# Kernel optimization log

Measured on AMD Instinct MI355X. Metric: run time of the kernel, lower is better.

The kernel has to match this reference:

```python
import jax, jax.numpy as jnp
import numpy as np

B, N, IN_DIM, OUT_DIM, H = 4, 2048, 128, 128, 4
NEG_SLOPE = 0.2


def setup_inputs() -> dict:
    key = jax.random.key(0)
    ks = jax.random.split(key, 6)
    # Xavier-ish scaling for stable softmax logits
    node_features = jax.random.normal(ks[0], (B, N, IN_DIM), dtype=jnp.float32)
    adjacency = jax.random.randint(ks[1], (B, N, N), 0, 2, dtype=jnp.int32)
    W = jax.random.normal(ks[2], (H, IN_DIM, OUT_DIM), dtype=jnp.float32) / np.sqrt(IN_DIM)
    a = jax.random.normal(ks[3], (H, 2 * OUT_DIM), dtype=jnp.float32) / np.sqrt(2 * OUT_DIM)
    out_proj_w = jax.random.normal(ks[4], (H * OUT_DIM, OUT_DIM), dtype=jnp.float32) / np.sqrt(H * OUT_DIM)
    out_proj_b = jax.random.normal(ks[5], (OUT_DIM,), dtype=jnp.float32) * 0.01
    return {"node_features": node_features, "adjacency": adjacency, "W": W,
            "a": a, "out_proj_w": out_proj_w, "out_proj_b": out_proj_b}


def reference(node_features, adjacency, W, a, out_proj_w, out_proj_b):
    D = W.shape[-1]
    # Per-head projection: h[b,h,n,o]
    h = jnp.einsum('bni,hio->bhno', node_features, W)
    # Additive attention score a^T [h_i || h_j] decomposed into src+dst parts
    # (exact since the score Linear has no bias).
    s = jnp.einsum('bhno,ho->bhn', h, a[:, :D])   # contribution of h_i
    d = jnp.einsum('bhno,ho->bhn', h, a[:, D:])   # contribution of h_j
    e = jax.nn.leaky_relu(s[..., :, None] + d[..., None, :], NEG_SLOPE)  # [B,H,N,N]
    e = jnp.where(adjacency[:, None, :, :] == 0, -jnp.inf, e)
    alpha = jax.nn.softmax(e, axis=-1)                                   # [B,H,N,N]
    out = jnp.einsum('bhnm,bhmo->bhno', alpha, h)                        # [B,H,N,D]
    b, nh, n, _ = out.shape
    cat = out.transpose(0, 2, 1, 3).reshape(b, n, nh * D)                # concat heads
    output = cat @ out_proj_w + out_proj_b                               # [B,N,D]
    return output, alpha
```

## Files before the change

kernel.cpp:

```cpp
#include <hip/hip_runtime.h>
#include <hip/hip_bf16.h>

#define BB 4
#define NN 2048
#define DD 128
#define HH 4
#define LOG2E 1.4426950408889634f
#define NEG_BIG (-1e30f)

typedef __attribute__((ext_vector_type(8))) short bf16x8;
typedef __attribute__((ext_vector_type(4))) short bf16x4;
typedef __attribute__((ext_vector_type(4))) float f32x4;
typedef __attribute__((ext_vector_type(8))) _Float16 f16x8;
typedef __attribute__((ext_vector_type(4))) _Float16 f16x4;

__device__ __forceinline__ unsigned short f2bf(float f) {
    union { float f; unsigned int u; } v; v.f = f;
    unsigned int r = v.u + 0x7FFF + ((v.u >> 16) & 1);
    return (unsigned short)(r >> 16);
}

__global__ __launch_bounds__(128) void k_prep(const float* __restrict__ W,
                                              const float* __restrict__ a,
                                              float* __restrict__ wsv,
                                              float* __restrict__ wdv,
                                              _Float16* __restrict__ WT16) {
    int h = blockIdx.x;
    int i = threadIdx.x;
    const float* Wr  = W + (h * DD + i) * DD;
    const float* as_ = a + h * 2 * DD;
    const float* ad_ = as_ + DD;
    float s = 0.f, d = 0.f;
    for (int o = 0; o < DD; ++o) {
        float w = Wr[o];
        s += w * as_[o];
        d += w * ad_[o];
        WT16[((size_t)h * DD + o) * DD + i] = (_Float16)w;
    }
    wsv[h * DD + i] = s;
    wdv[h * DD + i] = d;
}

__global__ __launch_bounds__(256) void k_sd(const float* __restrict__ x,
                                            const float* __restrict__ wsv,
                                            const float* __restrict__ wdv,
                                            float* __restrict__ s_out,
                                            float* __restrict__ d_out_) {
    __shared__ float xs[64 * 129];
    __shared__ float ws[4 * 129], wd[4 * 129];
    int tid = threadIdx.x;
    int b  = blockIdx.x / (NN / 64);
    int nb = (blockIdx.x % (NN / 64)) * 64;
    for (int idx = tid; idx < HH * DD; idx += 256) {
        ws[(idx >> 7) * 129 + (idx & 127)] = wsv[idx];
        wd[(idx >> 7) * 129 + (idx & 127)] = wdv[idx];
    }
    for (int idx = tid; idx < 64 * 128; idx += 256) {
        int r = idx >> 7, c = idx & 127;
        xs[r * 129 + c] = x[((size_t)b * NN + nb + r) * DD + c];
    }
    __syncthreads();
    int h = tid & 3, r = tid >> 2;
    float sv = 0.f, dv = 0.f;
#pragma unroll 8
    for (int i = 0; i < DD; ++i) {
        float xv = xs[r * 129 + i];
        sv += xv * ws[h * 129 + i];
        dv += xv * wd[h * 129 + i];
    }
    int n = nb + r;
    s_out[(b * HH + h) * NN + n] = sv;
    d_out_[(b * HH + h) * NN + n] = dv;
}

__global__ __launch_bounds__(256) void k_h_mfma(const float* __restrict__ x,
                                                const _Float16* __restrict__ WT16,
                                                unsigned short* __restrict__ hT) {
    __shared__ unsigned short wt_lds[128 * 128];
    __shared__ unsigned short x_lds[64 * 128];
    int tid = threadIdx.x;
    int bh = blockIdx.x >> 5;
    int nb = (blockIdx.x & 31) * 64;
    int b = bh >> 2, h = bh & 3;

    {
        int o = tid >> 1, ihalf = (tid & 1) * 64;
        const _Float16* src = WT16 + ((size_t)h * DD + o) * DD + ihalf;
#pragma unroll
        for (int q = 0; q < 8; ++q) {
            f16x8 v = *(const f16x8*)(src + q * 8);
            int byte = ((ihalf + q * 8) * 2) ^ ((o & 15) << 4);
            *(f16x8*)&wt_lds[o * 128 + (byte >> 1)] = v;
        }
    }
    {
        int n = tid >> 2, iseg = (tid & 3) * 32;
        const float* src = x + ((size_t)b * NN + nb + n) * DD + iseg;
#pragma unroll
        for (int q = 0; q < 8; ++q) {
            float4 v = *(const float4*)(src + q * 4);
            f16x4 p;
            p[0] = (_Float16)v.x; p[1] = (_Float16)v.y;
            p[2] = (_Float16)v.z; p[3] = (_Float16)v.w;
            int byte = ((iseg + q * 4) * 2) ^ ((n & 15) << 4);
            *(f16x4*)&x_lds[n * 128 + (byte >> 1)] = p;
        }
    }
    __syncthreads();

    int l = tid & 63, w = tid >> 6, col = l & 15, quad = l >> 4;
    f32x4 acc[8];
#pragma unroll
    for (int ot = 0; ot < 8; ++ot) acc[ot] = (f32x4){0.f, 0.f, 0.f, 0.f};
#pragma unroll
    for (int k = 0; k < 4; ++k) {
        int cbyte = (k * 64 + quad * 16) ^ (col << 4);
        f16x8 bv = *(const f16x8*)&x_lds[(w * 16 + col) * 128 + (cbyte >> 1)];
#pragma unroll
        for (int ot = 0; ot < 8; ++ot) {
            f16x8 av = *(const f16x8*)&wt_lds[(ot * 16 + col) * 128 + (cbyte >> 1)];
            acc[ot] = __builtin_amdgcn_mfma_f32_16x16x32_f16(av, bv, acc[ot], 0, 0, 0);
        }
    }
    unsigned short* base = hT + (size_t)bh * DD * NN;
#pragma unroll
    for (int ot = 0; ot < 8; ++ot)
#pragma unroll
        for (int r = 0; r < 4; ++r)
            base[(size_t)(ot * 16 + quad * 4 + r) * NN + nb + w * 16 + col] =
                f2bf(acc[ot][r]);
}

__global__ __launch_bounds__(256) void k_dmax(const float* __restrict__ d_,
                                              float* __restrict__ dmax_) {
    __shared__ float red[4];
    int bh = blockIdx.x, tid = threadIdx.x;
    const float4* dp = (const float4*)(d_ + (size_t)bh * NN);
    float4 v0 = dp[tid];
    float4 v1 = dp[256 + tid];
    float m = fmaxf(fmaxf(fmaxf(v0.x, v0.y), fmaxf(v0.z, v0.w)),
                    fmaxf(fmaxf(v1.x, v1.y), fmaxf(v1.z, v1.w)));
#pragma unroll
    for (int off = 32; off >= 1; off >>= 1)
        m = fmaxf(m, __shfl_xor(m, off, 64));
    if ((tid & 63) == 0) red[tid >> 6] = m;
    __syncthreads();
    if (tid == 0)
        dmax_[bh] = fmaxf(fmaxf(red[0], red[1]), fmaxf(red[2], red[3]));
}

struct AdjD {
    int4   a4[8];
    float4 d4;
};

__device__ __forceinline__ void adjd_load(int mb, const int* adj_base,
                                          const float* dg, int ac4, AdjD& R) {
#pragma unroll
    for (int p = 0; p < 8; ++p)
        R.a4[p] = *(const int4*)(adj_base + (size_t)(p * 8) * NN + mb);
    R.d4 = *(const float4*)(dg + mb + ac4);
}

__device__ __forceinline__ void p1_accum(const AdjD& R, const float (&sreg)[8],
                                         const float (&Mreg)[8], float (&Lp)[8]) {
#pragma unroll
    for (int p = 0; p < 8; ++p) {
        float sn = sreg[p], Mn = Mreg[p];
        float t0 = sn + R.d4.x, t1 = sn + R.d4.y;
        float t2 = sn + R.d4.z, t3 = sn + R.d4.w;
        float v0 = t0 > 0.f ? t0 : 0.2f * t0;
        float v1 = t1 > 0.f ? t1 : 0.2f * t1;
        float v2 = t2 > 0.f ? t2 : 0.2f * t2;
        float v3 = t3 > 0.f ? t3 : 0.2f * t3;
        float e0 = (R.a4[p].x != 0) ? exp2f((v0 - Mn) * LOG2E) : 0.f;
        float e1 = (R.a4[p].y != 0) ? exp2f((v1 - Mn) * LOG2E) : 0.f;
        float e2 = (R.a4[p].z != 0) ? exp2f((v2 - Mn) * LOG2E) : 0.f;
        float e3 = (R.a4[p].w != 0) ? exp2f((v3 - Mn) * LOG2E) : 0.f;
        Lp[p] += (e0 + e1) + (e2 + e3);
    }
}

template <bool WRITE_ALPHA>
__device__ __forceinline__ void attn_tile_body(
    int mb, AdjD& cur, AdjD& nxt,
    const int* adj_base, const float* dg, int ac4,
    const unsigned short* hbase,
    unsigned short* al_lds, unsigned short* hT_lds,
    const float (&sreg)[8], const float (&Mreg)[8], const float (&Lin)[8],
    float* alpha_base, int ar0, int hrow0, int hbyte,
    int w, int col, int quad, f32x4 (&acc)[8])
{
    bf16x8 hv[8];
#pragma unroll
    for (int q = 0; q < 8; ++q)
        hv[q] = *(const bf16x8*)(hbase + (size_t)(q * 16) * NN + mb);
    adjd_load((mb + 128) & (NN - 1), adj_base, dg, ac4, nxt);

#pragma unroll
    for (int p = 0; p < 8; ++p) {
        int row = p * 8 + ar0;
        float sn = sreg[p], Mn = Mreg[p], Li = Lin[p];
        float t0 = sn + cur.d4.x, t1 = sn + cur.d4.y;
        float t2 = sn + cur.d4.z, t3 = sn + cur.d4.w;
        float v0 = t0 > 0.f ? t0 : 0.2f * t0;
        float v1 = t1 > 0.f ? t1 : 0.2f * t1;
        float v2 = t2 > 0.f ? t2 : 0.2f * t2;
        float v3 = t3 > 0.f ? t3 : 0.2f * t3;
        float e0 = (cur.a4[p].x != 0) ? exp2f((v0 - Mn) * LOG2E) * Li : 0.f;
        float e1 = (cur.a4[p].y != 0) ? exp2f((v1 - Mn) * LOG2E) * Li : 0.f;
        float e2 = (cur.a4[p].z != 0) ? exp2f((v2 - Mn) * LOG2E) * Li : 0.f;
        float e3 = (cur.a4[p].w != 0) ? exp2f((v3 - Mn) * LOG2E) * Li : 0.f;
        bf16x4 pk;
        pk[0] = (short)f2bf(e0); pk[1] = (short)f2bf(e1);
        pk[2] = (short)f2bf(e2); pk[3] = (short)f2bf(e3);
        int abyte = (ac4 * 2) ^ ((row & 15) << 4);
        *(bf16x4*)&al_lds[row * 128 + (abyte >> 1)] = pk;
        if (WRITE_ALPHA) {
            float4 ev; ev.x = e0; ev.y = e1; ev.z = e2; ev.w = e3;
            *(float4*)(alpha_base + (size_t)(p * 8) * NN + mb) = ev;
        }
    }
#pragma unroll
    for (int q = 0; q < 8; ++q)
        *(bf16x8*)&hT_lds[(q * 16 + hrow0) * 128 + (hbyte >> 1)] = hv[q];

    __syncthreads();
#pragma unroll
    for (int k = 0; k < 4; ++k) {
        int cbyte = (k * 64 + quad * 16) ^ (col << 4);
        bf16x8 af = *(const bf16x8*)&al_lds[(w * 16 + col) * 128 + (cbyte >> 1)];
#pragma unroll
        for (int ot = 0; ot < 8; ++ot) {
            bf16x8 bfv = *(const bf16x8*)&hT_lds[(ot * 16 + col) * 128 + (cbyte >> 1)];
            acc[ot] = __builtin_amdgcn_mfma_f32_16x16x32_bf16(af, bfv, acc[ot], 0, 0, 0);
        }
    }
    __syncthreads();
}

template <bool WRITE_ALPHA>
__global__ __launch_bounds__(256) void k_attn_mfma(const int* __restrict__ adj,
                                                   const float* __restrict__ s_in,
                                                   const float* __restrict__ d_in_,
                                                   const float* __restrict__ dmax_,
                                                   const unsigned short* __restrict__ hT,
                                                   float* __restrict__ out_scr,
                                                   float* __restrict__ alpha_out,
                                                   float* __restrict__ Li_out) {
    __shared__ unsigned short al_lds[64 * 128];
    __shared__ unsigned short hT_lds[128 * 128];
    int tid = threadIdx.x;
    int bid = (int)(blockIdx.x & 7) * 64 + (int)(blockIdx.x >> 3);
    int bh = bid >> 5;
    int nb = (bid & 31) * 64;
    int b = bh >> 2;

    int ar0 = tid >> 5;
    int ac4 = (tid & 31) * 4;
    const int* adj_base = adj + ((size_t)b * NN + nb + ar0) * NN + ac4;
    float* alpha_base = WRITE_ALPHA
        ? alpha_out + ((size_t)bh * NN + nb + ar0) * NN + ac4 : nullptr;
    const float* dg = d_in_ + (size_t)bh * NN;

    float dmx = dmax_[bh];
    float sreg[8], Mreg[8];
#pragma unroll
    for (int p = 0; p < 8; ++p) {
        sreg[p] = s_in[bh * NN + nb + p * 8 + ar0];
        float t = sreg[p] + dmx;
        Mreg[p] = t > 0.f ? t : 0.2f * t;
    }

    float Lp[8];
#pragma unroll
    for (int p = 0; p < 8; ++p) Lp[p] = 0.f;
    {
        AdjD A0, A1;
        adjd_load(0, adj_base, dg, ac4, A0);
        for (int mb = 0; mb < NN; mb += 256) {
            adjd_load(mb + 128, adj_base, dg, ac4, A1);
            p1_accum(A0, sreg, Mreg, Lp);
            adjd_load((mb + 256) & (NN - 1), adj_base, dg, ac4, A0);
            p1_accum(A1, sreg, Mreg, Lp);
        }
    }
#pragma unroll
    for (int off = 16; off >= 1; off >>= 1)
#pragma unroll
        for (int p = 0; p < 8; ++p)
            Lp[p] += __shfl_xor(Lp[p], off, 64);
    float Lin[8];
#pragma unroll
    for (int p = 0; p < 8; ++p) Lin[p] = Lp[p] > 0.f ? 1.f / Lp[p] : 0.f;
    if (!WRITE_ALPHA && (tid & 31) == 0) {
#pragma unroll
        for (int p = 0; p < 8; ++p)
            Li_out[bh * NN + nb + p * 8 + ar0] = Lin[p];
    }

    int hrow0 = tid >> 4;
    int hcolu = (tid & 15) * 8;
    const unsigned short* hbase = hT + ((size_t)bh * DD + hrow0) * NN + hcolu;
    int hbyte = (hcolu * 2) ^ (hrow0 << 4);
    int l = tid & 63, w = tid >> 6, col = l & 15, quad = l >> 4;

    f32x4 acc[8];
#pragma unroll
    for (int ot = 0; ot < 8; ++ot) acc[ot] = (f32x4){0.f, 0.f, 0.f, 0.f};

    AdjD A0, A1;
    adjd_load(0, adj_base, dg, ac4, A0);

    for (int mb = 0; mb < NN; mb += 256) {
        attn_tile_body<WRITE_ALPHA>(mb, A0, A1, adj_base, dg, ac4, hbase,
                                    al_lds, hT_lds, sreg, Mreg, Lin,
                                    alpha_base, ar0, hrow0, hbyte,
                                    w, col, quad, acc);
        attn_tile_body<WRITE_ALPHA>(mb + 128, A1, A0, adj_base, dg, ac4, hbase,
                                    al_lds, hT_lds, sreg, Mreg, Lin,
                                    alpha_base, ar0, hrow0, hbyte,
                                    w, col, quad, acc);
    }
#pragma unroll
    for (int ot = 0; ot < 8; ++ot)
#pragma unroll
        for (int r = 0; r < 4; ++r)
            out_scr[((size_t)bh * NN + nb + w * 16 + quad * 4 + r) * DD + ot * 16 + col] =
                acc[ot][r];
}

__global__ __launch_bounds__(256) void k_proj(const float* __restrict__ out_scr,
                                              const float* __restrict__ Wp,
                                              const float* __restrict__ bias,
                                              float* __restrict__ out) {
    __shared__ float cs[16 * 512];
    int tid = threadIdx.x;
    int b  = blockIdx.x / (NN / 16);
    int nb = (blockIdx.x % (NN / 16)) * 16;
    for (int idx = tid; idx < 16 * 512; idx += 256) {
        int r = idx >> 9, c = idx & 511;
        int hh = c >> 7, oo = c & 127;
        cs[idx] = out_scr[((size_t)(b * HH + hh) * NN + nb + r) * DD + oo];
    }
    __syncthreads();
    int o = tid & 63, rg = tid >> 6;
    float bv0 = bias[o], bv1 = bias[o + 64];
    float acc0[4], acc1[4];
#pragma unroll
    for (int j = 0; j < 4; ++j) { acc0[j] = bv0; acc1[j] = bv1; }
    for (int k = 0; k < 512; k += 4) {
        float w00 = Wp[(k + 0) * DD + o], w01 = Wp[(k + 0) * DD + o + 64];
        float w10 = Wp[(k + 1) * DD + o], w11 = Wp[(k + 1) * DD + o + 64];
        float w20 = Wp[(k + 2) * DD + o], w21 = Wp[(k + 2) * DD + o + 64];
        float w30 = Wp[(k + 3) * DD + o], w31 = Wp[(k + 3) * DD + o + 64];
#pragma unroll
        for (int j = 0; j < 4; ++j) {
            float4 cq = *(const float4*)&cs[(rg * 4 + j) * 512 + k];
            acc0[j] += cq.x * w00 + cq.y * w10 + cq.z * w20 + cq.w * w30;
            acc1[j] += cq.x * w01 + cq.y * w11 + cq.z * w21 + cq.w * w31;
        }
    }
#pragma unroll
    for (int j = 0; j < 4; ++j) {
        out[((size_t)b * NN + nb + rg * 4 + j) * DD + o]      = acc0[j];
        out[((size_t)b * NN + nb + rg * 4 + j) * DD + o + 64] = acc1[j];
    }
}

__global__ __launch_bounds__(256) void k_alpha(const int* __restrict__ adj,
                                               const float* __restrict__ s_in,
                                               const float* __restrict__ d_in_,
                                               const float* __restrict__ dmax_,
                                               const float* __restrict__ Li_in,
                                               float* __restrict__ alpha_out) {
    int tid = threadIdx.x;
    int b = blockIdx.x / NN, n = blockIdx.x % NN;
    float sv[4], Mv[4], Lv[4];
#pragma unroll
    for (int h = 0; h < 4; ++h) {
        sv[h] = s_in[(b * HH + h) * NN + n];
        float t = sv[h] + dmax_[b * HH + h];
        Mv[h] = t > 0.f ? t : 0.2f * t;
        Lv[h] = Li_in[(b * HH + h) * NN + n];
    }
    const int* arow = adj + ((size_t)b * NN + n) * NN;
    for (int m = tid; m < NN; m += 256) {
        int av = arow[m];
#pragma unroll
        for (int h = 0; h < 4; ++h) {
            float val = 0.f;
            if (av != 0) {
                float t = sv[h] + d_in_[(b * HH + h) * NN + m];
                float v = t > 0.f ? t : 0.2f * t;
                val = exp2f((v - Mv[h]) * LOG2E) * Lv[h];
            }
            alpha_out[((size_t)(b * HH + h) * NN + n) * NN + m] = val;
        }
    }
}

extern "C" void kernel_launch(void* const* d_in, const int* in_sizes, int n_in,
                              void* d_out, int out_size, void* d_ws, size_t ws_size,
                              hipStream_t stream) {
    const float* x    = (const float*)d_in[0];
    const int*   adj  = (const int*)d_in[1];
    const float* W    = (const float*)d_in[2];
    const float* a    = (const float*)d_in[3];
    const float* Wp   = (const float*)d_in[4];
    const float* bias = (const float*)d_in[5];

    float* out       = (float*)d_out;
    float* alpha_out = out + (size_t)BB * NN * DD;

    float* ws    = (float*)d_ws;
    float* wsv   = ws;
    float* wdv   = wsv + HH * DD;
    float* s_    = wdv + HH * DD;
    float* d_    = s_ + (size_t)BB * HH * NN;
    float* Li_   = d_ + (size_t)BB * HH * NN;
    float* dmax_ = Li_ + (size_t)BB * HH * NN;
    _Float16* WT16 = (_Float16*)(dmax_ + 16);

    const size_t stats_bytes = (2 * HH * DD + 3 * (size_t)BB * HH * NN + 16) * sizeof(float)
                             + (size_t)HH * DD * DD * sizeof(_Float16);
    const size_t hT_bytes    = (size_t)BB * HH * NN * DD * sizeof(unsigned short);
    const size_t scr_bytes   = (size_t)BB * HH * NN * DD * sizeof(float);
    const bool fused = ws_size >= stats_bytes + hT_bytes + scr_bytes;

    unsigned short* hT;
    float* out_scr;
    if (fused) {
        hT      = (unsigned short*)((char*)d_ws + stats_bytes);
        out_scr = (float*)((char*)hT + hT_bytes);
    } else {
        hT      = (unsigned short*)alpha_out;
        out_scr = alpha_out + (size_t)BB * HH * NN * DD;
    }

    k_prep<<<HH, 128, 0, stream>>>(W, a, wsv, wdv, WT16);
    k_sd<<<BB * NN / 64, 256, 0, stream>>>(x, wsv, wdv, s_, d_);
    k_h_mfma<<<BB * HH * (NN / 64), 256, 0, stream>>>(x, WT16, hT);
    k_dmax<<<BB * HH, 256, 0, stream>>>(d_, dmax_);
    if (fused) {
        k_attn_mfma<true><<<BB * HH * (NN / 64), 256, 0, stream>>>(adj, s_, d_, dmax_,
                                                                   hT, out_scr, alpha_out, Li_);
        k_proj<<<BB * (NN / 16), 256, 0, stream>>>(out_scr, Wp, bias, out);
    } else {
        k_attn_mfma<false><<<BB * HH * (NN / 64), 256, 0, stream>>>(adj, s_, d_, dmax_,
                                                                    hT, out_scr, alpha_out, Li_);
        k_proj<<<BB * (NN / 16), 256, 0, stream>>>(out_scr, Wp, bias, out);
        k_alpha<<<BB * NN, 256, 0, stream>>>(adj, s_, d_, dmax_, Li_, alpha_out);
    }
}
```

Measured before the change: 444.7 us.

## Pack adjacency into bitmask once and read bits in attention kernel

Adds a pre-pass kernel that compresses the int32 adjacency matrix into one bit per entry, stored in workspace. The attention kernel's two passes (row-sum and alpha/MFMA) then read 32-bit mask words instead of int4 adjacency vectors, cutting the adjacency traffic that was previously read once per head and per pass. This costs one extra full read of the adjacency plus a small bitmask write, and a larger workspace requirement, which could drop the path into the non-fused fallback if the workspace is too small.

```diff
diff --git a/kernel.cpp b/kernel.cpp
--- a/kernel.cpp
+++ b/kernel.cpp
@@ -41,6 +41,22 @@
     wdv[h * DD + i] = d;
 }
 
+__global__ __launch_bounds__(256) void k_mask(const int* __restrict__ adj,
+                                              unsigned int* __restrict__ mbits) {
+    size_t w = (size_t)blockIdx.x * 256 + threadIdx.x;
+    const int* src = adj + w * 32;
+    unsigned int m = 0;
+#pragma unroll
+    for (int q = 0; q < 8; ++q) {
+        int4 a = *(const int4*)(src + q * 4);
+        m |= (a.x != 0 ? 1u : 0u) << (q * 4 + 0);
+        m |= (a.y != 0 ? 1u : 0u) << (q * 4 + 1);
+        m |= (a.z != 0 ? 1u : 0u) << (q * 4 + 2);
+        m |= (a.w != 0 ? 1u : 0u) << (q * 4 + 3);
+    }
+    mbits[w] = m;
+}
+
 __global__ __launch_bounds__(256) void k_sd(const float* __restrict__ x,
                                             const float* __restrict__ wsv,
                                             const float* __restrict__ wdv,
@@ -149,42 +165,45 @@
         dmax_[bh] = fmaxf(fmaxf(red[0], red[1]), fmaxf(red[2], red[3]));
 }
 
-struct AdjD {
-    int4   a4[8];
+struct MaskD {
+    unsigned int mw[8];
     float4 d4;
 };
 
-__device__ __forceinline__ void adjd_load(int mb, const int* adj_base,
-                                          const float* dg, int ac4, AdjD& R) {
+__device__ __forceinline__ void maskd_load(int mb, const unsigned int* mask_base,
+                                           const float* dg, int ac4, MaskD& R) {
+    int wo = mb >> 5;
 #pragma unroll
     for (int p = 0; p < 8; ++p)
-        R.a4[p] = *(const int4*)(adj_base + (size_t)(p * 8) * NN + mb);
+        R.mw[p] = mask_base[(size_t)(p * 8) * (NN / 32) + wo];
     R.d4 = *(const float4*)(dg + mb + ac4);
 }
 
-__device__ __forceinline__ void p1_accum(const AdjD& R, const float (&sreg)[8],
+__device__ __forceinline__ void p1_accum(const MaskD& R, int shift,
+                                         const float (&sreg)[8],
                                          const float (&Mreg)[8], float (&Lp)[8]) {
 #pragma unroll
     for (int p = 0; p < 8; ++p) {
         float sn = sreg[p], Mn = Mreg[p];
+        unsigned m4 = (R.mw[p] >> shift) & 0xFu;
         float t0 = sn + R.d4.x, t1 = sn + R.d4.y;
         float t2 = sn + R.d4.z, t3 = sn + R.d4.w;
         float v0 = t0 > 0.f ? t0 : 0.2f * t0;
         float v1 = t1 > 0.f ? t1 : 0.2f * t1;
         float v2 = t2 > 0.f ? t2 : 0.2f * t2;
         float v3 = t3 > 0.f ? t3 : 0.2f * t3;
-        float e0 = (R.a4[p].x != 0) ? exp2f((v0 - Mn) * LOG2E) : 0.f;
-        float e1 = (R.a4[p].y != 0) ? exp2f((v1 - Mn) * LOG2E) : 0.f;
-        float e2 = (R.a4[p].z != 0) ? exp2f((v2 - Mn) * LOG2E) : 0.f;
-        float e3 = (R.a4[p].w != 0) ? exp2f((v3 - Mn) * LOG2E) : 0.f;
+        float e0 = (m4 & 1u) ? exp2f((v0 - Mn) * LOG2E) : 0.f;
+        float e1 = (m4 & 2u) ? exp2f((v1 - Mn) * LOG2E) : 0.f;
+        float e2 = (m4 & 4u) ? exp2f((v2 - Mn) * LOG2E) : 0.f;
+        float e3 = (m4 & 8u) ? exp2f((v3 - Mn) * LOG2E) : 0.f;
         Lp[p] += (e0 + e1) + (e2 + e3);
     }
 }
 
 template <bool WRITE_ALPHA>
 __device__ __forceinline__ void attn_tile_body(
-    int mb, AdjD& cur, AdjD& nxt,
-    const int* adj_base, const float* dg, int ac4,
+    int mb, MaskD& cur, MaskD& nxt,
+    const unsigned int* mask_base, const float* dg, int ac4, int shift,
     const unsigned short* hbase,
     unsigned short* al_lds, unsigned short* hT_lds,
     const float (&sreg)[8], const float (&Mreg)[8], const float (&Lin)[8],
@@ -195,22 +214,23 @@
 #pragma unroll
     for (int q = 0; q < 8; ++q)
         hv[q] = *(const bf16x8*)(hbase + (size_t)(q * 16) * NN + mb);
-    adjd_load((mb + 128) & (NN - 1), adj_base, dg, ac4, nxt);
+    maskd_load((mb + 128) & (NN - 1), mask_base, dg, ac4, nxt);
 
 #pragma unroll
     for (int p = 0; p < 8; ++p) {
         int row = p * 8 + ar0;
         float sn = sreg[p], Mn = Mreg[p], Li = Lin[p];
+        unsigned m4 = (cur.mw[p] >> shift) & 0xFu;
         float t0 = sn + cur.d4.x, t1 = sn + cur.d4.y;
         float t2 = sn + cur.d4.z, t3 = sn + cur.d4.w;
         float v0 = t0 > 0.f ? t0 : 0.2f * t0;
         float v1 = t1 > 0.f ? t1 : 0.2f * t1;
         float v2 = t2 > 0.f ? t2 : 0.2f * t2;
         float v3 = t3 > 0.f ? t3 : 0.2f * t3;
-        float e0 = (cur.a4[p].x != 0) ? exp2f((v0 - Mn) * LOG2E) * Li : 0.f;
-        float e1 = (cur.a4[p].y != 0) ? exp2f((v1 - Mn) * LOG2E) * Li : 0.f;
-        float e2 = (cur.a4[p].z != 0) ? exp2f((v2 - Mn) * LOG2E) * Li : 0.f;
-        float e3 = (cur.a4[p].w != 0) ? exp2f((v3 - Mn) * LOG2E) * Li : 0.f;
+        float e0 = (m4 & 1u) ? exp2f((v0 - Mn) * LOG2E) * Li : 0.f;
+        float e1 = (m4 & 2u) ? exp2f((v1 - Mn) * LOG2E) * Li : 0.f;
+        float e2 = (m4 & 4u) ? exp2f((v2 - Mn) * LOG2E) * Li : 0.f;
+        float e3 = (m4 & 8u) ? exp2f((v3 - Mn) * LOG2E) * Li : 0.f;
         bf16x4 pk;
         pk[0] = (short)f2bf(e0); pk[1] = (short)f2bf(e1);
         pk[2] = (short)f2bf(e2); pk[3] = (short)f2bf(e3);
@@ -240,7 +260,7 @@
 }
 
 template <bool WRITE_ALPHA>
-__global__ __launch_bounds__(256) void k_attn_mfma(const int* __restrict__ adj,
+__global__ __launch_bounds__(256) void k_attn_mfma(const unsigned int* __restrict__ mbits,
                                                    const float* __restrict__ s_in,
                                                    const float* __restrict__ d_in_,
                                                    const float* __restrict__ dmax_,
@@ -258,7 +278,9 @@
 
     int ar0 = tid >> 5;
     int ac4 = (tid & 31) * 4;
-    const int* adj_base = adj + ((size_t)b * NN + nb + ar0) * NN + ac4;
+    int shift = ac4 & 31;
+    const unsigned int* mask_base =
+        mbits + ((size_t)b * NN + nb + ar0) * (NN / 32) + (ac4 >> 5);
     float* alpha_base = WRITE_ALPHA
         ? alpha_out + ((size_t)bh * NN + nb + ar0) * NN + ac4 : nullptr;
     const float* dg = d_in_ + (size_t)bh * NN;
@@ -276,13 +298,13 @@
 #pragma unroll
     for (int p = 0; p < 8; ++p) Lp[p] = 0.f;
     {
-        AdjD A0, A1;
-        adjd_load(0, adj_base, dg, ac4, A0);
+        MaskD A0, A1;
+        maskd_load(0, mask_base, dg, ac4, A0);
         for (int mb = 0; mb < NN; mb += 256) {
-            adjd_load(mb + 128, adj_base, dg, ac4, A1);
-            p1_accum(A0, sreg, Mreg, Lp);
-            adjd_load((mb + 256) & (NN - 1), adj_base, dg, ac4, A0);
-            p1_accum(A1, sreg, Mreg, Lp);
+            maskd_load(mb + 128, mask_base, dg, ac4, A1);
+            p1_accum(A0, shift, sreg, Mreg, Lp);
+            maskd_load((mb + 256) & (NN - 1), mask_base, dg, ac4, A0);
+            p1_accum(A1, shift, sreg, Mreg, Lp);
         }
     }
 #pragma unroll
@@ -309,15 +331,15 @@
 #pragma unroll
     for (int ot = 0; ot < 8; ++ot) acc[ot] = (f32x4){0.f, 0.f, 0.f, 0.f};
 
-    AdjD A0, A1;
-    adjd_load(0, adj_base, dg, ac4, A0);
+    MaskD A0, A1;
+    maskd_load(0, mask_base, dg, ac4, A0);
 
     for (int mb = 0; mb < NN; mb += 256) {
-        attn_tile_body<WRITE_ALPHA>(mb, A0, A1, adj_base, dg, ac4, hbase,
+        attn_tile_body<WRITE_ALPHA>(mb, A0, A1, mask_base, dg, ac4, shift, hbase,
                                     al_lds, hT_lds, sreg, Mreg, Lin,
                                     alpha_base, ar0, hrow0, hbyte,
                                     w, col, quad, acc);
-        attn_tile_body<WRITE_ALPHA>(mb + 128, A1, A0, adj_base, dg, ac4, hbase,
+        attn_tile_body<WRITE_ALPHA>(mb + 128, A1, A0, mask_base, dg, ac4, shift, hbase,
                                     al_lds, hT_lds, sreg, Mreg, Lin,
                                     alpha_base, ar0, hrow0, hbyte,
                                     w, col, quad, acc);
@@ -421,9 +443,12 @@
     float* Li_   = d_ + (size_t)BB * HH * NN;
     float* dmax_ = Li_ + (size_t)BB * HH * NN;
     _Float16* WT16 = (_Float16*)(dmax_ + 16);
-
+    unsigned int* mbits = (unsigned int*)(WT16 + (size_t)HH * DD * DD);
+
+    const size_t mask_bytes  = (size_t)BB * NN * NN / 8;
     const size_t stats_bytes = (2 * HH * DD + 3 * (size_t)BB * HH * NN + 16) * sizeof(float)
-                             + (size_t)HH * DD * DD * sizeof(_Float16);
+                             + (size_t)HH * DD * DD * sizeof(_Float16)
+                             + mask_bytes;
     const size_t hT_bytes    = (size_t)BB * HH * NN * DD * sizeof(unsigned short);
     const size_t scr_bytes   = (size_t)BB * HH * NN * DD * sizeof(float);
     const bool fused = ws_size >= stats_bytes + hT_bytes + scr_bytes;
@@ -439,15 +464,16 @@
     }
 
     k_prep<<<HH, 128, 0, stream>>>(W, a, wsv, wdv, WT16);
+    k_mask<<<BB * NN * NN / 32 / 256, 256, 0, stream>>>(adj, mbits);
     k_sd<<<BB * NN / 64, 256, 0, stream>>>(x, wsv, wdv, s_, d_);
     k_h_mfma<<<BB * HH * (NN / 64), 256, 0, stream>>>(x, WT16, hT);
     k_dmax<<<BB * HH, 256, 0, stream>>>(d_, dmax_);
     if (fused) {
-        k_attn_mfma<true><<<BB * HH * (NN / 64), 256, 0, stream>>>(adj, s_, d_, dmax_,
+        k_attn_mfma<true><<<BB * HH * (NN / 64), 256, 0, stream>>>(mbits, s_, d_, dmax_,
                                                                    hT, out_scr, alpha_out, Li_);
         k_proj<<<BB * (NN / 16), 256, 0, stream>>>(out_scr, Wp, bias, out);
     } else {
-        k_attn_mfma<false><<<BB * HH * (NN / 64), 256, 0, stream>>>(adj, s_, d_, dmax_,
+        k_attn_mfma<false><<<BB * HH * (NN / 64), 256, 0, stream>>>(mbits, s_, d_, dmax_,
                                                                     hT, out_scr, alpha_out, Li_);
         k_proj<<<BB * (NN / 16), 256, 0, stream>>>(out_scr, Wp, bias, out);
         k_alpha<<<BB * NN, 256, 0, stream>>>(adj, s_, d_, dmax_, Li_, alpha_out);
```

Result: slower. 458.0 us (+3.0%).
